# Optimization experiments

Hardware: AMD Instinct MI355X
Metric: run time of the kernel (lower is better)

## Reference

```python
import jax, jax.numpy as jnp
import numpy as np

B, S, H = 2, 1024, 4096
NH, NKV, D = 32, 8, 128
EPS = 1e-6
THETA = 10000.0


def rotate_half(x):
    x1, x2 = jnp.split(x, 2, axis=-1)
    return jnp.concatenate([-x2, x1], axis=-1)


def rmsnorm(x, w, eps):
    # RMSNorm over the last (head_dim) axis
    var = jnp.mean(x * x, axis=-1, keepdims=True)
    return x * jax.lax.rsqrt(var + eps) * w


def setup_inputs() -> dict:
    key = jax.random.key(0)
    ks = jax.random.split(key, 6)
    hidden_states = jax.random.normal(ks[0], (B, S, H), dtype=jnp.float32)
    # scaled init so activations stay O(1)
    Wq = jax.random.normal(ks[1], (NH * D, H), dtype=jnp.float32) * (H ** -0.5)
    Wk = jax.random.normal(ks[2], (NKV * D, H), dtype=jnp.float32) * (H ** -0.5)
    Wv = jax.random.normal(ks[3], (NKV * D, H), dtype=jnp.float32) * (H ** -0.5)
    Wo = jax.random.normal(ks[4], (H, NH * D), dtype=jnp.float32) * ((NH * D) ** -0.5)
    q_norm_w = jnp.ones((D,), dtype=jnp.float32)
    k_norm_w = jnp.ones((D,), dtype=jnp.float32)
    # standard default RoPE cos/sin tables, broadcast to [B, S, D]
    pos = jnp.arange(S, dtype=jnp.float32)
    inv_freq = 1.0 / (THETA ** (jnp.arange(0, D, 2, dtype=jnp.float32) / D))
    freqs = pos[:, None] * inv_freq[None, :]            # [S, D/2]
    emb = jnp.concatenate([freqs, freqs], axis=-1)      # [S, D]
    cos = jnp.broadcast_to(jnp.cos(emb)[None], (B, S, D)).astype(jnp.float32)
    sin = jnp.broadcast_to(jnp.sin(emb)[None], (B, S, D)).astype(jnp.float32)
    return dict(hidden_states=hidden_states, cos=cos, sin=sin,
                Wq=Wq, Wk=Wk, Wv=Wv, Wo=Wo,
                q_norm_w=q_norm_w, k_norm_w=k_norm_w)


def reference(hidden_states, cos, sin, Wq, Wk, Wv, Wo, q_norm_w, k_norm_w):
    b, s, h = hidden_states.shape
    # fused QKV projections (MojoLinear: y = x @ W.T, no bias)
    q = (hidden_states @ Wq.T).reshape(b, s, NH, D)
    k = (hidden_states @ Wk.T).reshape(b, s, NKV, D)
    v = (hidden_states @ Wv.T).reshape(b, s, NKV, D)
    # per-head-dim RMSNorm on q and k, then [B, H, S, D] layout
    q = rmsnorm(q, q_norm_w, EPS).transpose(0, 2, 1, 3)   # [B, NH,  S, D]
    k = rmsnorm(k, k_norm_w, EPS).transpose(0, 2, 1, 3)   # [B, NKV, S, D]
    v = v.transpose(0, 2, 1, 3)                           # [B, NKV, S, D]
    # RoPE (rotate-half)
    c = cos[:, None, :, :]
    sn = sin[:, None, :, :]
    q = q * c + rotate_half(q) * sn
    k = k * c + rotate_half(k) * sn
    # GQA: expand KV heads to query heads
    groups = NH // NKV
    k = jnp.repeat(k, groups, axis=1)                     # [B, NH, S, D]
    v = jnp.repeat(v, groups, axis=1)
    # causal attention (prefill with empty paged cache == causal SDPA)
    scores = jnp.einsum('bhqd,bhkd->bhqk', q, k) * (D ** -0.5)
    causal = jnp.tril(jnp.ones((s, s), dtype=bool))
    scores = jnp.where(causal, scores, jnp.finfo(scores.dtype).min)
    probs = jax.nn.softmax(scores, axis=-1)
    out = jnp.einsum('bhqk,bhkd->bhqd', probs, v)         # [B, NH, S, D]
    out = out.transpose(0, 2, 1, 3).reshape(b, s, NH * D)
    return out @ Wo.T
```

## Files before the change

kernel.cpp:

```cpp
#include <hip/hip_runtime.h>


typedef float  f32x4   __attribute__((ext_vector_type(4)));
typedef float  f32x16  __attribute__((ext_vector_type(16)));
typedef __bf16 bf16x8  __attribute__((ext_vector_type(8)));
typedef unsigned short u16x8 __attribute__((ext_vector_type(8)));

__device__ __forceinline__ unsigned short f2b(float f) {
    union { float f; unsigned int u; } x;
    x.f = f;
    unsigned int u = x.u;
    unsigned int r = u + 0x7fffu + ((u >> 16) & 1u);
    return (unsigned short)(r >> 16);
}

__device__ __forceinline__ void async16(const unsigned short* g, unsigned short* l) {
    __builtin_amdgcn_global_load_lds(
        (const __attribute__((address_space(1))) void*)g,
        (__attribute__((address_space(3))) void*)l, 16, 0, 0);
}

__global__ __launch_bounds__(256) void cvt_all(const float* __restrict__ hsrc,
                                               const float* __restrict__ wq,
                                               const float* __restrict__ wk,
                                               const float* __restrict__ wv,
                                               const float* __restrict__ wo,
                                               unsigned short* __restrict__ hidb,
                                               unsigned short* __restrict__ wqkvb,
                                               unsigned short* __restrict__ wob) {
    int i = blockIdx.x * 256 + threadIdx.x;
    if (i >= 6291456) return;
    const float* s; unsigned short* d; int j;
    if (i < 1048576)      { s = hsrc; d = hidb;             j = i; }
    else if (i < 3145728) { s = wq;   d = wqkvb;            j = i - 1048576; }
    else if (i < 3670016) { s = wk;   d = wqkvb + 16777216; j = i - 3145728; }
    else if (i < 4194304) { s = wv;   d = wqkvb + 20971520; j = i - 3670016; }
    else                  { s = wo;   d = wob;              j = i - 4194304; }
    const float4* s4 = (const float4*)s + (size_t)j * 2;
    float4 a = s4[0], b = s4[1];
    u16x8 o;
    o[0] = f2b(a.x); o[1] = f2b(a.y); o[2] = f2b(a.z); o[3] = f2b(a.w);
    o[4] = f2b(b.x); o[5] = f2b(b.y); o[6] = f2b(b.z); o[7] = f2b(b.w);
    *((u16x8*)d + j) = o;
}

__global__ __launch_bounds__(512, 2) void gemm256_bt(const unsigned short* __restrict__ A,
                                                     const unsigned short* __restrict__ W,
                                                     float* __restrict__ C,
                                                     int K, int N) {
    __shared__ __align__(16) unsigned short Ab[3][256 * 64];
    __shared__ __align__(16) unsigned short Bb[2][192 * 64];

    const int tid  = threadIdx.x;
    const int wave = tid >> 6, lane = tid & 63;
    const int wm   = wave >> 2, wn = wave & 3;
    const int l15  = lane & 15, h = lane >> 4;
    const int cx0  = (h ^ (l15 & 7)) << 3;
    const int cx1  = cx0 ^ 32;
    const int stgrow = wave * 8 + (lane >> 3);
    const int stgcol = ((lane & 7) ^ (lane >> 3)) << 3;
    const int aRow0 = blockIdx.y * 256;
    const int bRow0 = blockIdx.x * 192;
    const int NT = K >> 6;

#define STAGE_A(t, s, bi) async16(A + (size_t)(aRow0 + (s)*64 + stgrow) * K + (t)*64 + stgcol, \
                                  &Ab[bi][(s)*4096 + wave*512])
#define STAGE_B(t, s, bi) async16(W + (size_t)(bRow0 + (s)*64 + stgrow) * K + (t)*64 + stgcol, \
                                  &Bb[bi][(s)*4096 + wave*512])
#define RD_AQ(dst, buf, q) do { \
    _Pragma("unroll") \
    for (int mi = 0; mi < 2; mi++) { \
        const unsigned short* ap_ = (buf) + (wm * 128 + (q) * 32 + mi * 16 + l15) * 64; \
        dst[mi][0] = *(const bf16x8*)(ap_ + cx0); \
        dst[mi][1] = *(const bf16x8*)(ap_ + cx1); \
    } } while (0)
#define RD_B(dst, buf) do { \
    _Pragma("unroll") \
    for (int nf = 0; nf < 3; nf++) { \
        const unsigned short* bp_ = (buf) + (wn * 48 + nf * 16 + l15) * 64; \
        dst[nf][0] = *(const bf16x8*)(bp_ + cx0); \
        dst[nf][1] = *(const bf16x8*)(bp_ + cx1); \
    } } while (0)
#define MFMA_Q(q, AR, BR) do { \
    _Pragma("unroll") \
    for (int mi = 0; mi < 2; mi++) \
    _Pragma("unroll") \
    for (int nf = 0; nf < 3; nf++) { \
        acc[(q)*2+mi][nf] = __builtin_amdgcn_mfma_f32_16x16x32_bf16(AR[mi][0], BR[nf][0], acc[(q)*2+mi][nf], 0, 0, 0); \
        acc[(q)*2+mi][nf] = __builtin_amdgcn_mfma_f32_16x16x32_bf16(AR[mi][1], BR[nf][1], acc[(q)*2+mi][nf], 0, 0, 0); \
    } } while (0)
#define SB()      __builtin_amdgcn_sched_barrier(0)
#define BARRIER() __builtin_amdgcn_s_barrier()
#define PRIO1()   __builtin_amdgcn_s_setprio(1)
#define PRIO0()   __builtin_amdgcn_s_setprio(0)
#define LGKM(n)   asm volatile("s_waitcnt lgkmcnt(" #n ")" ::: "memory")

#define TILE(T, BC, BN_) do { \
    const int t_ = (T); \
    const unsigned short* Ab_  = Ab[t_ % 3]; \
    const unsigned short* AbN_ = Ab[(t_ + 1) % 3]; \
    const unsigned short* BbN_ = Bb[(t_ + 1) & 1]; \
    const int rb1 = (t_ & 1) ^ 1, ra2 = (t_ + 2) % 3; \
    const bool sb = (t_ + 1 < NT), sa = (t_ + 2 < NT); \
     \
    RD_AQ(rB, Ab_, 1); \
    if (sb) { STAGE_B(t_ + 1, 0, rb1); STAGE_B(t_ + 1, 1, rb1); } \
    SB(); BARRIER(); LGKM(4); SB(); \
    PRIO1(); MFMA_Q(0, rA, BC); PRIO0(); SB(); BARRIER(); \
     \
    RD_AQ(rC, Ab_, 2); \
    if (sb) STAGE_B(t_ + 1, 2, rb1); \
    if (sa) STAGE_A(t_ + 2, 0, ra2); \
    SB(); BARRIER(); LGKM(4); SB(); \
    PRIO1(); MFMA_Q(1, rB, BC); PRIO0(); SB(); BARRIER(); \
     \
    RD_AQ(rD, Ab_, 3); \
    if (sa) { STAGE_A(t_ + 2, 1, ra2); STAGE_A(t_ + 2, 2, ra2); \
              asm volatile("s_waitcnt vmcnt(3)" ::: "memory"); } \
    else    { asm volatile("s_waitcnt vmcnt(0)" ::: "memory"); } \
    SB(); BARRIER(); LGKM(4); SB(); \
    PRIO1(); MFMA_Q(2, rC, BC); PRIO0(); SB(); BARRIER(); \
     \
    if (sb) { RD_AQ(rA, AbN_, 0); RD_B(BN_, BbN_); } \
    if (sa) STAGE_A(t_ + 2, 3, ra2); \
    SB(); BARRIER(); \
    if (sb) { LGKM(10); } else { LGKM(0); } \
    SB(); \
    PRIO1(); MFMA_Q(3, rD, BC); PRIO0(); SB(); BARRIER(); \
} while (0)

    f32x4 acc[8][3] = {};
    bf16x8 rA[2][2], rB[2][2], rC[2][2], rD[2][2];
    bf16x8 bc[3][2], bn[3][2];

    STAGE_B(0, 0, 0); STAGE_B(0, 1, 0); STAGE_B(0, 2, 0);
    STAGE_A(0, 0, 0); STAGE_A(0, 1, 0); STAGE_A(0, 2, 0); STAGE_A(0, 3, 0);
    STAGE_A(1, 0, 1); STAGE_A(1, 1, 1); STAGE_A(1, 2, 1); STAGE_A(1, 3, 1);
    asm volatile("s_waitcnt vmcnt(4)" ::: "memory");
    SB(); BARRIER(); SB();
    RD_B(bc, Bb[0]);
    RD_AQ(rA, Ab[0], 0);
    SB();

    for (int t = 0; t < NT; t += 2) {
        TILE(t,     bc, bn);
        TILE(t + 1, bn, bc);
    }

    #pragma unroll
    for (int mf = 0; mf < 8; mf++)
        #pragma unroll
        for (int nf = 0; nf < 3; nf++)
            #pragma unroll
            for (int r = 0; r < 4; r++) {
                int row = aRow0 + wm * 128 + mf * 16 + h * 4 + r;
                int col = bRow0 + wn * 48 + nf * 16 + l15;
                C[(size_t)row * N + col] = acc[mf][nf][r];
            }
#undef STAGE_A
#undef STAGE_B
#undef RD_AQ
#undef RD_B
#undef MFMA_Q
#undef SB
#undef BARRIER
#undef PRIO1
#undef PRIO0
#undef LGKM
#undef TILE
}

__global__ __launch_bounds__(256) void gemm_bt_bf16(const unsigned short* __restrict__ A,
                                                    const unsigned short* __restrict__ W,
                                                    float* __restrict__ C,
                                                    int K, int N) {
    __shared__ __align__(16) unsigned short As[128 * 64];
    __shared__ __align__(16) unsigned short Bs[128 * 64];

    const int tid  = threadIdx.x;
    const int wave = tid >> 6, lane = tid & 63;
    const int wm   = wave >> 1, wn = wave & 1;
    const int l31  = lane & 31, lh = lane >> 5;
    const int arow = blockIdx.y * 128, brow = blockIdx.x * 128;

    int rr[4], gc[4], slot[4];
    #pragma unroll
    for (int it = 0; it < 4; it++) {
        slot[it] = it * 4 + wave;
        int ci = slot[it] * 64 + lane;
        rr[it] = ci >> 3;
        int c  = ci & 7;
        gc[it] = c ^ (rr[it] & 7);
    }

    f32x16 acc[2][2] = {};

    for (int k0 = 0; k0 < K; k0 += 64) {
        #pragma unroll
        for (int it = 0; it < 4; it++) {
            async16(A + (size_t)(arow + rr[it]) * K + k0 + gc[it] * 8, &As[slot[it] * 512]);
            async16(W + (size_t)(brow + rr[it]) * K + k0 + gc[it] * 8, &Bs[slot[it] * 512]);
        }
        __syncthreads();

        bf16x8 af[4][2], bfr[4][2];
        #pragma unroll
        for (int ks = 0; ks < 4; ks++) {
            #pragma unroll
            for (int i = 0; i < 2; i++) {
                int rowa = wm * 64 + i * 32 + l31;
                int ch   = (ks * 2 + lh) ^ (rowa & 7);
                af[ks][i]  = *(const bf16x8*)&As[rowa * 64 + ch * 8];
                int rowb = wn * 64 + i * 32 + l31;
                int chb  = (ks * 2 + lh) ^ (rowb & 7);
                bfr[ks][i] = *(const bf16x8*)&Bs[rowb * 64 + chb * 8];
            }
        }
        #pragma unroll
        for (int ks = 0; ks < 4; ks++)
            #pragma unroll
            for (int i = 0; i < 2; i++)
                #pragma unroll
                for (int j = 0; j < 2; j++)
                    acc[i][j] = __builtin_amdgcn_mfma_f32_32x32x16_bf16(af[ks][i], bfr[ks][j], acc[i][j], 0, 0, 0);
        __syncthreads();
    }

    #pragma unroll
    for (int i = 0; i < 2; i++)
        #pragma unroll
        for (int j = 0; j < 2; j++)
            #pragma unroll
            for (int r = 0; r < 16; r++) {
                int row = arow + wm * 64 + i * 32 + lh * 4 + (r & 3) + 8 * (r >> 2);
                int col = brow + wn * 64 + j * 32 + l31;
                C[(size_t)row * N + col] = acc[i][j][r];
            }
}

__global__ __launch_bounds__(256) void norm_rope(const float* __restrict__ X, int rstride,
                                                 const float* __restrict__ cosp,
                                                 const float* __restrict__ sinp,
                                                 const float* __restrict__ w,
                                                 unsigned short* __restrict__ Y, int nh) {
    const int wid  = blockIdx.x * 4 + (threadIdx.x >> 6);
    const int lane = threadIdx.x & 63;
    const int row  = wid / nh;
    const int h    = wid - row * nh;

    const float* xp = X + (size_t)row * rstride + h * 128;
    float x0 = xp[lane], x1 = xp[lane + 64];
    float ss = x0 * x0 + x1 * x1;
    #pragma unroll
    for (int off = 32; off; off >>= 1) ss += __shfl_xor(ss, off, 64);
    float r = rsqrtf(ss * (1.0f / 128.0f) + 1e-6f);
    float n0 = x0 * r * w[lane];
    float n1 = x1 * r * w[lane + 64];
    const float* cp = cosp + (size_t)row * 128;
    const float* sp = sinp + (size_t)row * 128;
    float y0 = n0 * cp[lane]      - n1 * sp[lane];
    float y1 = n1 * cp[lane + 64] + n0 * sp[lane + 64];
    const int b = row >> 10, s = row & 1023;
    unsigned short* yp = Y + (((size_t)(b * nh + h)) * 1024 + s) * 128;
    yp[lane]      = f2b(y0);
    yp[lane + 64] = f2b(y1);
}

__global__ __launch_bounds__(256) void v_trans(const float* __restrict__ V,
                                               unsigned short* __restrict__ Vt) {
    __shared__ float T[64][65];
    const int tid = threadIdx.x;
    const int st = blockIdx.x >> 1, dt = blockIdx.x & 1;
    const int bh = blockIdx.y, b = bh >> 3, h = bh & 7;

    const int sl = tid >> 2, c0 = (tid & 3) * 16;
    const float* src = V + (size_t)(b * 1024 + st * 64 + sl) * 6144 + h * 128 + dt * 64 + c0;
    #pragma unroll
    for (int j = 0; j < 4; j++) {
        float4 v = *(const float4*)(src + j * 4);
        *(float4*)&T[sl][c0 + j * 4] = v;
    }
    __syncthreads();

    const int dgrp = tid >> 6, sl2 = tid & 63;
    unsigned short* dst = Vt + (size_t)bh * 131072 + st * 64 + sl2;
    #pragma unroll
    for (int jd = 0; jd < 16; jd++) {
        int dl = dgrp * 16 + jd;
        dst[(size_t)(dt * 64 + dl) * 1024] = f2b(T[sl2][dl]);
    }
}

__global__ __launch_bounds__(256) void attn(const unsigned short* __restrict__ Qb,
                                            const unsigned short* __restrict__ Kb,
                                            const unsigned short* __restrict__ Vt,
                                            unsigned short* __restrict__ Ob) {
    __shared__ __align__(16) unsigned short Klds[128 * 128];
    __shared__ __align__(16) unsigned short Plds[4][16][136];

    const int tid  = threadIdx.x;
    const int w    = tid >> 6, lane = tid & 63;
    const int quad = lane >> 4, l15 = lane & 15;
    const int h = blockIdx.y, b = blockIdx.z, kvh = h >> 2;

    const unsigned short* Qp = Qb + ((size_t)(b * 32 + h))   * 131072;
    const unsigned short* Kp = Kb + ((size_t)(b * 8 + kvh))  * 131072;
    const unsigned short* Vp = Vt + ((size_t)(b * 8 + kvh))  * 131072;
    const float c2 = (float)(0.08838834764831845 * 1.4426950408889634);

    for (int half = 0; half < 2; half++) {
        const int qt = half ? (15 - (int)blockIdx.x) : (int)blockIdx.x;
        const int q0 = qt * 64;
        const int qrow = q0 + w * 16 + l15;

        bf16x8 qf[4];
        #pragma unroll
        for (int ks = 0; ks < 4; ks++)
            qf[ks] = *(const bf16x8*)(Qp + (size_t)qrow * 128 + ks * 32 + quad * 8);

        float m_i[4], l_i[4];
        #pragma unroll
        for (int r = 0; r < 4; r++) { m_i[r] = -1e30f; l_i[r] = 0.0f; }
        f32x4 o[8] = {};

        const int ntiles = (qt >> 1) + 1;
        const int nfull  = (qt * 64 + 1) >> 7;

        for (int kt = 0; kt < ntiles; kt++) {
            __syncthreads();
            #pragma unroll
            for (int it = 0; it < 8; it++) {
                int slot = it * 4 + w;
                int ci = slot * 64 + lane;
                int r = ci >> 4, c = ci & 15;
                int g = (c & 8) | ((c ^ r) & 7);
                async16(Kp + (size_t)(kt * 128 + r) * 128 + g * 8, &Klds[slot * 512]);
            }
            __syncthreads();

            f32x4 sacc[8] = {};
            __builtin_amdgcn_s_setprio(1);
            #pragma unroll
            for (int ks = 0; ks < 4; ks++) {
                #pragma unroll
                for (int tn = 0; tn < 8; tn++) {
                    int row = tn * 16 + l15;
                    int ch  = ks * 4 + quad;
                    int chs = (ch & 8) | ((ch ^ row) & 7);
                    bf16x8 kf = *(const bf16x8*)&Klds[row * 128 + chs * 8];
                    sacc[tn] = __builtin_amdgcn_mfma_f32_16x16x32_bf16(qf[ks], kf, sacc[tn], 0, 0, 0);
                }
            }
            __builtin_amdgcn_s_setprio(0);

            const bool masked = (kt >= nfull);
            #pragma unroll
            for (int r = 0; r < 4; r++) {
                float sv[8];
                float rmax = -1e30f;
                if (masked) {
                    const int qg = q0 + w * 16 + quad * 4 + r;
                    #pragma unroll
                    for (int tn = 0; tn < 8; tn++) {
                        float v = sacc[tn][r];
                        int kg = kt * 128 + tn * 16 + l15;
                        if (kg > qg) v = -1e30f;
                        sv[tn] = v;
                        rmax = fmaxf(rmax, v);
                    }
                } else {
                    #pragma unroll
                    for (int tn = 0; tn < 8; tn++) {
                        sv[tn] = sacc[tn][r];
                        rmax = fmaxf(rmax, sv[tn]);
                    }
                }
                #pragma unroll
                for (int off = 8; off; off >>= 1) rmax = fmaxf(rmax, __shfl_xor(rmax, off, 16));
                float mnew  = fmaxf(m_i[r], rmax);
                float alpha = __builtin_amdgcn_exp2f((m_i[r] - mnew) * c2);
                float rsum  = 0.0f;
                #pragma unroll
                for (int tn = 0; tn < 8; tn++) {
                    float p = __builtin_amdgcn_exp2f((sv[tn] - mnew) * c2);
                    sv[tn] = p;
                    rsum += p;
                }
                #pragma unroll
                for (int off = 8; off; off >>= 1) rsum += __shfl_xor(rsum, off, 16);
                m_i[r] = mnew;
                l_i[r] = l_i[r] * alpha + rsum;
                #pragma unroll
                for (int td = 0; td < 8; td++) o[td][r] *= alpha;
                #pragma unroll
                for (int tn = 0; tn < 8; tn++)
                    Plds[w][quad * 4 + r][tn * 16 + l15] = f2b(sv[tn]);
            }

            __builtin_amdgcn_s_setprio(1);
            #pragma unroll
            for (int ks = 0; ks < 4; ks++) {
                bf16x8 pf = *(const bf16x8*)&Plds[w][l15][ks * 32 + quad * 8];
                #pragma unroll
                for (int td = 0; td < 8; td++) {
                    bf16x8 vf = *(const bf16x8*)(Vp + (size_t)(td * 16 + l15) * 1024 + kt * 128 + ks * 32 + quad * 8);
                    o[td] = __builtin_amdgcn_mfma_f32_16x16x32_bf16(pf, vf, o[td], 0, 0, 0);
                }
            }
            __builtin_amdgcn_s_setprio(0);
        }

        #pragma unroll
        for (int r = 0; r < 4; r++) {
            float inv = 1.0f / l_i[r];
            const int qg = q0 + w * 16 + quad * 4 + r;
            unsigned short* op = Ob + ((size_t)(b * 1024 + qg)) * 4096 + h * 128;
            #pragma unroll
            for (int td = 0; td < 8; td++)
                op[td * 16 + l15] = f2b(o[td][r] * inv);
        }
    }
}

extern "C" void kernel_launch(void* const* d_in, const int* in_sizes, int n_in,
                              void* d_out, int out_size, void* d_ws, size_t ws_size,
                              hipStream_t stream) {
    const float* hid  = (const float*)d_in[0];
    const float* cosp = (const float*)d_in[1];
    const float* sinp = (const float*)d_in[2];
    const float* Wq   = (const float*)d_in[3];
    const float* Wk   = (const float*)d_in[4];
    const float* Wv   = (const float*)d_in[5];
    const float* Wo   = (const float*)d_in[6];
    const float* qw   = (const float*)d_in[7];
    const float* kw   = (const float*)d_in[8];
    float* out = (float*)d_out;

    char* ws = (char*)d_ws;
    float* QKVf = (float*)ws;
    unsigned short* Ob = (unsigned short*)ws;
    size_t off = (size_t)2048 * 6144 * 4;
    unsigned short* hidb  = (unsigned short*)(ws + off); off += (size_t)2048 * 4096 * 2;
    unsigned short* Wqkvb = (unsigned short*)(ws + off); off += (size_t)6144 * 4096 * 2;
    unsigned short* Wob   = (unsigned short*)(ws + off);
    unsigned short* Qb    = hidb;
    unsigned short* Kb    = Wqkvb;
    unsigned short* Vt    = Wqkvb + (size_t)2048 * 1024;

    dim3 blk(256);
    cvt_all<<<24576, blk, 0, stream>>>(hid, Wq, Wk, Wv, Wo, hidb, Wqkvb, Wob);
    gemm256_bt<<<dim3(32, 8), dim3(512), 0, stream>>>(hidb, Wqkvb, QKVf, 4096, 6144);
    norm_rope<<<16384, blk, 0, stream>>>(QKVf,        6144, cosp, sinp, qw, Qb, 32);
    norm_rope<<<4096,  blk, 0, stream>>>(QKVf + 4096, 6144, cosp, sinp, kw, Kb, 8);
    v_trans<<<dim3(32, 16), blk, 0, stream>>>(QKVf + 5120, Vt);
    attn<<<dim3(8, 32, 2), blk, 0, stream>>>(Qb, Kb, Vt, Ob);
    gemm_bt_bf16<<<dim3(32, 16), blk, 0, stream>>>(Ob, Wob, out, 4096, 4096);
}
```

Before: 513.4 us.

## Cut per-quarter barriers in QKV GEMM main loop and regroup async staging

Removes the workgroup barriers between the four MFMA quarters of each K-tile in the QKV projection GEMM, keeping a single barrier per tile before the next tile's LDS fragments are read. Global-to-LDS staging is regrouped: all three B sub-tiles are issued in the first quarter and the A sub-tiles in pairs, with a single vmcnt wait before the barrier. K and N become compile-time constants. The goal is less wave synchronisation overhead and more freedom for waves to drift, at the cost of relying on buffer rotation alone to prevent LDS read/write races.

```diff
diff --git a/kernel.cpp b/kernel.cpp
--- a/kernel.cpp
+++ b/kernel.cpp
@@ -46,8 +46,8 @@
 
 __global__ __launch_bounds__(512, 2) void gemm256_bt(const unsigned short* __restrict__ A,
                                                      const unsigned short* __restrict__ W,
-                                                     float* __restrict__ C,
-                                                     int K, int N) {
+                                                     float* __restrict__ C) {
+    constexpr int K = 4096, N = 6144;
     __shared__ __align__(16) unsigned short Ab[3][256 * 64];
     __shared__ __align__(16) unsigned short Bb[2][192 * 64];
 
@@ -97,36 +97,33 @@
 
 #define TILE(T, BC, BN_) do { \
     const int t_ = (T); \
-    const unsigned short* Ab_  = Ab[t_ % 3]; \
-    const unsigned short* AbN_ = Ab[(t_ + 1) % 3]; \
-    const unsigned short* BbN_ = Bb[(t_ + 1) & 1]; \
+    const unsigned short* Ab_ = Ab[t_ % 3]; \
     const int rb1 = (t_ & 1) ^ 1, ra2 = (t_ + 2) % 3; \
     const bool sb = (t_ + 1 < NT), sa = (t_ + 2 < NT); \
      \
     RD_AQ(rB, Ab_, 1); \
-    if (sb) { STAGE_B(t_ + 1, 0, rb1); STAGE_B(t_ + 1, 1, rb1); } \
-    SB(); BARRIER(); LGKM(4); SB(); \
-    PRIO1(); MFMA_Q(0, rA, BC); PRIO0(); SB(); BARRIER(); \
+    if (sb) { STAGE_B(t_ + 1, 0, rb1); STAGE_B(t_ + 1, 1, rb1); STAGE_B(t_ + 1, 2, rb1); } \
+    SB(); LGKM(4); SB(); \
+    PRIO1(); MFMA_Q(0, rA, BC); PRIO0(); SB(); \
      \
     RD_AQ(rC, Ab_, 2); \
-    if (sb) STAGE_B(t_ + 1, 2, rb1); \
-    if (sa) STAGE_A(t_ + 2, 0, ra2); \
-    SB(); BARRIER(); LGKM(4); SB(); \
-    PRIO1(); MFMA_Q(1, rB, BC); PRIO0(); SB(); BARRIER(); \
+    if (sa) { STAGE_A(t_ + 2, 0, ra2); STAGE_A(t_ + 2, 1, ra2); } \
+    SB(); LGKM(4); SB(); \
+    PRIO1(); MFMA_Q(1, rB, BC); PRIO0(); SB(); \
      \
     RD_AQ(rD, Ab_, 3); \
-    if (sa) { STAGE_A(t_ + 2, 1, ra2); STAGE_A(t_ + 2, 2, ra2); \
-              asm volatile("s_waitcnt vmcnt(3)" ::: "memory"); } \
-    else    { asm volatile("s_waitcnt vmcnt(0)" ::: "memory"); } \
-    SB(); BARRIER(); LGKM(4); SB(); \
-    PRIO1(); MFMA_Q(2, rC, BC); PRIO0(); SB(); BARRIER(); \
+    if (sa) { STAGE_A(t_ + 2, 2, ra2); STAGE_A(t_ + 2, 3, ra2); } \
+    SB(); LGKM(4); SB(); \
+    PRIO1(); MFMA_Q(2, rC, BC); PRIO0(); SB(); \
      \
-    if (sb) { RD_AQ(rA, AbN_, 0); RD_B(BN_, BbN_); } \
-    if (sa) STAGE_A(t_ + 2, 3, ra2); \
-    SB(); BARRIER(); \
+    if (sa) asm volatile("s_waitcnt vmcnt(4)" ::: "memory"); \
+    else    asm volatile("s_waitcnt vmcnt(0)" ::: "memory"); \
+    SB(); BARRIER(); SB(); \
+    if (sb) { RD_B(BN_, Bb[(t_ + 1) & 1]); RD_AQ(rA, Ab[(t_ + 1) % 3], 0); } \
+    SB(); \
     if (sb) { LGKM(10); } else { LGKM(0); } \
     SB(); \
-    PRIO1(); MFMA_Q(3, rD, BC); PRIO0(); SB(); BARRIER(); \
+    PRIO1(); MFMA_Q(3, rD, BC); PRIO0(); SB(); \
 } while (0)
 
     f32x4 acc[8][3] = {};
@@ -449,7 +446,7 @@
 
     dim3 blk(256);
     cvt_all<<<24576, blk, 0, stream>>>(hid, Wq, Wk, Wv, Wo, hidb, Wqkvb, Wob);
-    gemm256_bt<<<dim3(32, 8), dim3(512), 0, stream>>>(hidb, Wqkvb, QKVf, 4096, 6144);
+    gemm256_bt<<<dim3(32, 8), dim3(512), 0, stream>>>(hidb, Wqkvb, QKVf);
     norm_rope<<<16384, blk, 0, stream>>>(QKVf,        6144, cosp, sinp, qw, Qb, 32);
     norm_rope<<<4096,  blk, 0, stream>>>(QKVf + 4096, 6144, cosp, sinp, kw, Kb, 8);
     v_trans<<<dim3(32, 16), blk, 0, stream>>>(QKVf + 5120, Vt);
```

New measurement: 503.8 us. About the same (-1.9%).
